# Performance work log

Measured on AMD Instinct MI355X. Metric: run time of the kernel, lower is better.

## Reference

```python
import jax, jax.numpy as jnp
import numpy as np

N = 32768
D_IN = 1728   # 192*3*3
D = 1024
C_CLS = 2


def setup_inputs() -> dict:
    key = jax.random.key(0)
    ks = jax.random.split(key, 8)
    # _initialize_weights: Linear weights ~ N(0, 0.01), biases zero
    x = jax.random.normal(ks[0], (N, D_IN), dtype=jnp.float32)
    w1 = jax.random.normal(ks[1], (D, D_IN), dtype=jnp.float32) * 0.01
    b1 = jnp.zeros((D,), jnp.float32)
    w2 = jax.random.normal(ks[2], (D, D), dtype=jnp.float32) * 0.01
    b2 = jnp.zeros((D,), jnp.float32)
    w_fc = jax.random.normal(ks[3], (C_CLS, D), dtype=jnp.float32) * 0.01
    b_fc = jnp.zeros((C_CLS,), jnp.float32)
    w_q = jax.random.normal(ks[4], (D, D), dtype=jnp.float32) * 0.01
    b_q = jnp.zeros((D,), jnp.float32)
    w_v = jax.random.normal(ks[5], (D, D), dtype=jnp.float32) * 0.01
    b_v = jnp.zeros((D,), jnp.float32)
    # Conv1d(2,2,kernel_size=1024): weight [out=2, in=2, k=1024]
    fan = C_CLS * D
    w_fcc = jax.random.uniform(ks[6], (C_CLS, C_CLS, D), jnp.float32,
                               -1.0 / np.sqrt(fan), 1.0 / np.sqrt(fan))
    b_fcc = jax.random.uniform(ks[7], (C_CLS,), jnp.float32,
                               -1.0 / np.sqrt(fan), 1.0 / np.sqrt(fan))
    return {"x": x, "w1": w1, "b1": b1, "w2": w2, "b2": b2,
            "w_fc": w_fc, "b_fc": b_fc, "w_q": w_q, "b_q": b_q,
            "w_v": w_v, "b_v": b_v, "w_fcc": w_fcc, "b_fcc": b_fcc}


def reference(x, w1, b1, w2, b2, w_fc, b_fc, w_q, b_q, w_v, b_v, w_fcc, b_fcc):
    # classifier MLP (dropout = identity in eval)
    h = jax.nn.relu(x @ w1.T + b1)          # [N, 1024]
    feat = jax.nn.relu(h @ w2.T + b2)       # [N, 1024]
    instance_pred = feat @ w_fc.T + b_fc    # [N, 2]
    V = feat @ w_v.T + b_v                  # [N, 1024]
    Q = feat @ w_q.T + b_q                  # [N, 1024]
    # torch.sort(..., descending=True)[1][0] == argmax per class column
    top_idx = jnp.argmax(instance_pred, axis=0)   # [2]
    m_feats = feat[top_idx]                 # [2, 1024]
    q_max = m_feats @ w_q.T + b_q           # [2, 1024]
    scale = jnp.sqrt(jnp.float32(Q.shape[1]))
    A = jax.nn.softmax((Q @ q_max.T) / scale, axis=0)  # softmax over instances, [N, 2]
    B = A.T @ V                             # [2, 1024]
    # Conv1d(2,2,k=1024) over length-1024 input -> single output position
    C = (jnp.einsum('oik,ik->o', w_fcc, B) + b_fcc).reshape(1, C_CLS)
    return instance_pred, C, A, B[None]
```

## Files before the change

### kernel.cpp

```cpp
#include <hip/hip_runtime.h>
#include <stdint.h>


typedef unsigned short u16;
typedef __attribute__((ext_vector_type(8))) short short8;
typedef __attribute__((ext_vector_type(4))) float floatx4;

#define TILE 128
#define BK 32

__device__ __forceinline__ float bf2f(u16 u) {
  union { unsigned u; float f; } x; x.u = ((unsigned)u) << 16; return x.f;
}
__device__ __forceinline__ u16 f2bf(float f) {
  union { float f; unsigned u; } x; x.f = f;
  return (u16)((x.u + 0x7fffu + ((x.u >> 16) & 1u)) >> 16);
}
__device__ __forceinline__ unsigned ordf(float f) {
  union { float f; unsigned u; } x; x.f = f;
  return (x.u & 0x80000000u) ? ~x.u : (x.u | 0x80000000u);
}
__device__ __forceinline__ void gload16(const void* g, void* l) {
  __builtin_amdgcn_global_load_lds(
      (const __attribute__((address_space(1))) void*)g,
      (__attribute__((address_space(3))) void*)l, 16, 0, 0);
}

template <int MODE>
__global__ __launch_bounds__(256) void gemm_bt(
    const u16* __restrict__ A, const u16* __restrict__ B,
    const float* __restrict__ bias, u16* __restrict__ O,
    float* __restrict__ OL, int K, int ntiles, int ldo) {
  __shared__ __align__(16) u16 SH[16384];

  const int xcd = blockIdx.x & 7;
  const int j = blockIdx.x >> 3;
  const int mstride = gridDim.x / (ntiles << 3);
  const int mt = xcd * mstride + j / ntiles;
  const int nt = j % ntiles;
  const int m0 = mt * TILE, n0 = nt * TILE;
  const int tid = threadIdx.x;
  const int lane = tid & 63;
  const int wm = (tid >> 7) * 64;
  const int wn = ((tid >> 6) & 1) * 64;

  floatx4 acc[4][4];
#pragma unroll
  for (int i = 0; i < 4; ++i)
#pragma unroll
    for (int jf = 0; jf < 4; ++jf) acc[i][jf] = (floatx4){0.f, 0.f, 0.f, 0.f};

  const int srow = tid >> 2;
  const int sq = ((tid & 3) - srow) & 3;
  const u16* Ag0 = A + (size_t)(m0 + srow) * K + sq * 8;
  const u16* Ag1 = Ag0 + (size_t)64 * K;
  const u16* Bg0 = B + (size_t)(n0 + srow) * K + sq * 8;
  const u16* Bg1 = Bg0 + (size_t)64 * K;
  u16* const ASl[2] = {SH + tid * 8, SH + 4096 + tid * 8};
  u16* const BSl[2] = {SH + 8192 + tid * 8, SH + 12288 + tid * 8};

  const int fr = lane & 15;
  const int fq = lane >> 4;
  const int fo = (size_t)0;
  const u16* const AF[2] = {
      SH + (wm + fr) * BK + (((fq + fr) & 3) * 8),
      SH + 4096 + (wm + fr) * BK + (((fq + fr) & 3) * 8)};
  const u16* const BF[2] = {
      SH + 8192 + (wn + fr) * BK + (((fq + fr) & 3) * 8),
      SH + 12288 + (wn + fr) * BK + (((fq + fr) & 3) * 8)};
  (void)fo;

  gload16(Ag0, ASl[0]); gload16(Ag1, ASl[0] + 2048);
  gload16(Bg0, BSl[0]); gload16(Bg1, BSl[0] + 2048);
  Ag0 += BK; Ag1 += BK; Bg0 += BK; Bg1 += BK;

  const int kiters = K / BK;
  for (int kt = 0; kt < kiters; ++kt) {
    const int cur = kt & 1, nxt = cur ^ 1;
    __syncthreads();
    if (kt + 1 < kiters) {
      gload16(Ag0, ASl[nxt]); gload16(Ag1, ASl[nxt] + 2048);
      gload16(Bg0, BSl[nxt]); gload16(Bg1, BSl[nxt] + 2048);
      Ag0 += BK; Ag1 += BK; Bg0 += BK; Bg1 += BK;
    }
    short8 a[4], b[4];
#pragma unroll
    for (int f = 0; f < 4; ++f) {
      a[f] = *(const short8*)(AF[cur] + f * 16 * BK);
      b[f] = *(const short8*)(BF[cur] + f * 16 * BK);
    }
#pragma unroll
    for (int i = 0; i < 4; ++i)
#pragma unroll
      for (int jf = 0; jf < 4; ++jf)
        acc[i][jf] = __builtin_amdgcn_mfma_f32_16x16x32_bf16(a[i], b[jf],
                                                             acc[i][jf], 0, 0, 0);
  }

  const int er = fq * 4;
  const int ec = fr;
  if (MODE == 1 && n0 >= 1024) {
    if (wn == 0 && ec < 2) {
#pragma unroll
      for (int i = 0; i < 4; ++i) {
        const int row = m0 + wm + i * 16 + er;
#pragma unroll
        for (int r = 0; r < 4; ++r)
          OL[(size_t)(row + r) * 2 + ec] = acc[i][0][r];
      }
    }
    return;
  }

  __syncthreads();
#pragma unroll
  for (int jf = 0; jf < 4; ++jf) {
    const int col = wn + jf * 16 + ec;
    const float bv = bias[n0 + col];
#pragma unroll
    for (int i = 0; i < 4; ++i) {
      const int row = wm + i * 16 + er;
#pragma unroll
      for (int r = 0; r < 4; ++r) {
        float v = acc[i][jf][r] + bv;
        if (MODE == 0) v = fmaxf(v, 0.f);
        SH[(row + r) * TILE + col] = f2bf(v);
      }
    }
  }
  __syncthreads();
#pragma unroll
  for (int c = 0; c < 8; ++c) {
    const int flat = c * 256 + tid;
    const int row = flat >> 4, ch = flat & 15;
    short8 v = *(const short8*)(SH + flat * 8);
    *(short8*)(O + (size_t)(m0 + row) * ldo + n0 + ch * 8) = v;
  }
}

__global__ void k_prep(const float* __restrict__ x, const float* __restrict__ w1,
                       const float* __restrict__ w2, const float* __restrict__ wv,
                       u16* __restrict__ XB, u16* __restrict__ W1B,
                       u16* __restrict__ W2B, u16* __restrict__ B3,
                       float* __restrict__ Bbuf, unsigned long long* __restrict__ keys) {
  int b = blockIdx.x;
  const int tid = threadIdx.x;
  const float* s; u16* d;
  if (b < 55296) { s = x; d = XB; }
  else if ((b -= 55296) < 1728) { s = w1; d = W1B; }
  else if ((b -= 1728) < 1024) { s = w2; d = W2B; }
  else if ((b -= 1024) < 1024) { s = wv; d = B3; }
  else {
    b -= 1024;
    int i = b * 256 + tid;
    if (i < 129024) B3[1026 * 1024 + i] = 0;
    if (i < 2048) Bbuf[i] = 0.f;
    if (i < 2) keys[i] = 0ull;
    return;
  }
  int i = b * 256 + tid;
  float4 v = ((const float4*)s)[i];
  unsigned long long o = (unsigned long long)f2bf(v.x) |
                         ((unsigned long long)f2bf(v.y) << 16) |
                         ((unsigned long long)f2bf(v.z) << 32) |
                         ((unsigned long long)f2bf(v.w) << 48);
  ((unsigned long long*)d)[i] = o;
}

__global__ __launch_bounds__(256) void k_ip(const u16* __restrict__ feat,
                                            const float* __restrict__ wfc,
                                            const float* __restrict__ bfc,
                                            float* __restrict__ out_ip) {
  const int row = blockIdx.x * 4 + (threadIdx.x >> 6);
  const int lane = threadIdx.x & 63;
  const u16* fr = feat + (size_t)row * 1024 + lane * 16;
  const float* w0 = wfc + lane * 16;
  const float* w1 = wfc + 1024 + lane * 16;
  float s0 = 0.f, s1 = 0.f;
#pragma unroll
  for (int t = 0; t < 16; ++t) {
    float f = bf2f(fr[t]);
    s0 += f * w0[t];
    s1 += f * w1[t];
  }
#pragma unroll
  for (int off = 32; off > 0; off >>= 1) {
    s0 += __shfl_down(s0, off, 64);
    s1 += __shfl_down(s1, off, 64);
  }
  if (lane == 0) {
    out_ip[(size_t)row * 2 + 0] = s0 + bfc[0];
    out_ip[(size_t)row * 2 + 1] = s1 + bfc[1];
  }
}

__global__ __launch_bounds__(256) void k_argmax(const float* __restrict__ ip,
                                                unsigned long long* __restrict__ keys) {
  float m0 = -1e30f, m1 = -1e30f;
  int i0 = 0, i1 = 0;
  for (int i = blockIdx.x * 256 + threadIdx.x; i < 32768; i += 256 * 64) {
    float v0 = ip[2 * i], v1 = ip[2 * i + 1];
    if (v0 > m0) { m0 = v0; i0 = i; }
    if (v1 > m1) { m1 = v1; i1 = i; }
  }
  unsigned long long k0 =
      ((unsigned long long)ordf(m0) << 32) | (0xFFFFFFFFu - (unsigned)i0);
  unsigned long long k1 =
      ((unsigned long long)ordf(m1) << 32) | (0xFFFFFFFFu - (unsigned)i1);
#pragma unroll
  for (int off = 32; off > 0; off >>= 1) {
    unsigned long long t0 = __shfl_down(k0, off, 64);
    unsigned long long t1 = __shfl_down(k1, off, 64);
    if (t0 > k0) k0 = t0;
    if (t1 > k1) k1 = t1;
  }
  __shared__ unsigned long long s0[4], s1[4];
  const int lane = threadIdx.x & 63, wv = threadIdx.x >> 6;
  if (lane == 0) { s0[wv] = k0; s1[wv] = k1; }
  __syncthreads();
  if (threadIdx.x == 0) {
    for (int w = 1; w < 4; ++w) {
      if (s0[w] > k0) k0 = s0[w];
      if (s1[w] > k1) k1 = s1[w];
    }
    atomicMax(keys + 0, k0);
    atomicMax(keys + 1, k1);
  }
}

__global__ __launch_bounds__(256) void k_qmax(const u16* __restrict__ feat,
                                              const float* __restrict__ wq,
                                              const float* __restrict__ bq,
                                              const unsigned long long* __restrict__ keys,
                                              float* __restrict__ qmax) {
  const int gw = blockIdx.x * 4 + (threadIdx.x >> 6);
  const int c = gw >> 10, k = gw & 1023;
  const int lane = threadIdx.x & 63;
  const int idx = (int)(0xFFFFFFFFu - (unsigned)(keys[c] & 0xFFFFFFFFull));
  const u16* fr = feat + (size_t)idx * 1024 + lane * 16;
  const float* wr = wq + (size_t)k * 1024 + lane * 16;
  float s = 0.f;
#pragma unroll
  for (int t = 0; t < 16; ++t) s += bf2f(fr[t]) * wr[t];
#pragma unroll
  for (int off = 32; off > 0; off >>= 1) s += __shfl_down(s, off, 64);
  if (lane == 0) qmax[c * 1024 + k] = s + bq[k];
}

__global__ __launch_bounds__(256) void k_t(const float* __restrict__ wq,
                                           const float* __restrict__ qmax,
                                           float* __restrict__ tpart) {
  const int jb = blockIdx.x & 3, kp = blockIdx.x >> 2;
  const int jcol = jb * 256 + threadIdx.x;
  float s0 = 0.f, s1 = 0.f;
  for (int k = kp * 128; k < kp * 128 + 128; ++k) {
    float w = wq[(size_t)k * 1024 + jcol];
    s0 += qmax[k] * w;
    s1 += qmax[1024 + k] * w;
  }
  tpart[kp * 2048 + jcol] = s0;
  tpart[kp * 2048 + 1024 + jcol] = s1;
}

__global__ __launch_bounds__(256) void k_tcast(const float* __restrict__ tpart,
                                               u16* __restrict__ b3) {
  const int i = blockIdx.x * 256 + threadIdx.x;
  float s = 0.f;
#pragma unroll
  for (int kp = 0; kp < 8; ++kp) s += tpart[kp * 2048 + i];
  b3[(size_t)(1024 + (i >> 10)) * 1024 + (i & 1023)] = f2bf(s);
}

__global__ __launch_bounds__(256) void k_reduce(const float* __restrict__ lg,
                                                float* __restrict__ ms) {
  __shared__ float r0[256], r1[256];
  const int tid = threadIdx.x;
  float m0 = -1e30f, m1 = -1e30f;
  for (int i = tid; i < 32768; i += 256) {
    m0 = fmaxf(m0, lg[2 * i]);
    m1 = fmaxf(m1, lg[2 * i + 1]);
  }
  r0[tid] = m0; r1[tid] = m1;
  __syncthreads();
  for (int s = 128; s > 0; s >>= 1) {
    if (tid < s) {
      r0[tid] = fmaxf(r0[tid], r0[tid + s]);
      r1[tid] = fmaxf(r1[tid], r1[tid + s]);
    }
    __syncthreads();
  }
  m0 = r0[0]; m1 = r1[0];
  __syncthreads();
  float s0 = 0.f, s1 = 0.f;
  for (int i = tid; i < 32768; i += 256) {
    s0 += __expf((lg[2 * i] - m0) * 0.03125f);
    s1 += __expf((lg[2 * i + 1] - m1) * 0.03125f);
  }
  r0[tid] = s0; r1[tid] = s1;
  __syncthreads();
  for (int s = 128; s > 0; s >>= 1) {
    if (tid < s) { r0[tid] += r0[tid + s]; r1[tid] += r1[tid + s]; }
    __syncthreads();
  }
  if (tid == 0) { ms[0] = m0; ms[1] = m1; ms[2] = r0[0]; ms[3] = r1[0]; }
}

__global__ __launch_bounds__(256) void k_ab(const float* __restrict__ lg,
                                            const float* __restrict__ ms,
                                            const u16* __restrict__ V,
                                            float* __restrict__ outA,
                                            float* __restrict__ Bbuf) {
  const int tid = threadIdx.x;
  const int row0 = blockIdx.x * 128;
  const float m0 = ms[0], m1 = ms[1];
  const float inv0 = 1.f / ms[2], inv1 = 1.f / ms[3];
  {
    const int r = row0 + (tid >> 1);
    const int c = tid & 1;
    outA[2 * r + c] =
        __expf((lg[2 * r + c] - (c ? m1 : m0)) * 0.03125f) * (c ? inv1 : inv0);
  }
  float p0[4] = {0, 0, 0, 0}, p1[4] = {0, 0, 0, 0};
  const int kb = tid * 4;
  for (int r = row0; r < row0 + 128; ++r) {
    const float a0 = __expf((lg[2 * r] - m0) * 0.03125f) * inv0;
    const float a1 = __expf((lg[2 * r + 1] - m1) * 0.03125f) * inv1;
    unsigned long long vv = *(const unsigned long long*)(V + (size_t)r * 1024 + kb);
    float f0 = bf2f((u16)vv), f1 = bf2f((u16)(vv >> 16));
    float f2 = bf2f((u16)(vv >> 32)), f3 = bf2f((u16)(vv >> 48));
    p0[0] += a0 * f0; p0[1] += a0 * f1; p0[2] += a0 * f2; p0[3] += a0 * f3;
    p1[0] += a1 * f0; p1[1] += a1 * f1; p1[2] += a1 * f2; p1[3] += a1 * f3;
  }
#pragma unroll
  for (int t = 0; t < 4; ++t) {
    atomicAdd(&Bbuf[kb + t], p0[t]);
    atomicAdd(&Bbuf[1024 + kb + t], p1[t]);
  }
}

__global__ __launch_bounds__(256) void k_c(const float* __restrict__ Bbuf,
                                           const float* __restrict__ wfcc,
                                           const float* __restrict__ bfcc,
                                           float* __restrict__ outC,
                                           float* __restrict__ outB) {
  __shared__ float r0[256], r1[256];
  const int tid = threadIdx.x;
  float s0 = 0.f, s1 = 0.f;
  for (int i = tid; i < 2048; i += 256) {
    float b = Bbuf[i];
    outB[i] = b;
    s0 += wfcc[i] * b;
    s1 += wfcc[2048 + i] * b;
  }
  r0[tid] = s0; r1[tid] = s1;
  __syncthreads();
  for (int s = 128; s > 0; s >>= 1) {
    if (tid < s) { r0[tid] += r0[tid + s]; r1[tid] += r1[tid + s]; }
    __syncthreads();
  }
  if (tid == 0) {
    outC[0] = r0[0] + bfcc[0];
    outC[1] = r1[0] + bfcc[1];
  }
}

extern "C" void kernel_launch(void* const* d_in, const int* in_sizes, int n_in,
                              void* d_out, int out_size, void* d_ws, size_t ws_size,
                              hipStream_t stream) {
  const float* x    = (const float*)d_in[0];
  const float* w1   = (const float*)d_in[1];
  const float* b1   = (const float*)d_in[2];
  const float* w2   = (const float*)d_in[3];
  const float* b2   = (const float*)d_in[4];
  const float* wfc  = (const float*)d_in[5];
  const float* bfc  = (const float*)d_in[6];
  const float* wq   = (const float*)d_in[7];
  const float* bq   = (const float*)d_in[8];
  const float* wv   = (const float*)d_in[9];
  const float* bv   = (const float*)d_in[10];
  const float* wfcc = (const float*)d_in[11];
  const float* bfcc = (const float*)d_in[12];

  float* out   = (float*)d_out;
  float* outIP = out;
  float* outC  = out + 65536;
  float* outA  = out + 65538;
  float* outB  = out + 131074;

  char* ws = (char*)d_ws;
  u16* XB  = (u16*)(ws);
  u16* HB  = (u16*)(ws + 113246208);
  u16* FB  = (u16*)(ws + 180355072);
  u16* W1B = (u16*)(ws + 247463936);
  float* TPART = (float*)(ws + 247463936);
  u16* W2B = (u16*)(ws + 251002880);
  u16* B3  = (u16*)(ws + 253100032);
  float* LG = (float*)(ws + 255459328);
  float* QM = (float*)(ws + 255721472);
  unsigned long long* KEYS = (unsigned long long*)(ws + 255729664);
  float* MS   = (float*)(ws + 255729680);
  float* BBUF = (float*)(ws + 255729696);

  k_prep<<<55296 + 1728 + 1024 + 1024 + 505, 256, 0, stream>>>(
      x, w1, w2, wv, XB, W1B, W2B, B3, BBUF, KEYS);

  gemm_bt<0><<<256 * 8, 256, 0, stream>>>(XB, W1B, b1, HB, nullptr, 1728, 8, 1024);
  gemm_bt<0><<<256 * 8, 256, 0, stream>>>(HB, W2B, b2, FB, nullptr, 1024, 8, 1024);

  k_ip<<<8192, 256, 0, stream>>>(FB, wfc, bfc, outIP);
  k_argmax<<<64, 256, 0, stream>>>(outIP, KEYS);
  k_qmax<<<512, 256, 0, stream>>>(FB, wq, bq, KEYS, QM);
  k_t<<<32, 256, 0, stream>>>(wq, QM, TPART);
  k_tcast<<<8, 256, 0, stream>>>(TPART, B3);

  gemm_bt<1><<<256 * 9, 256, 0, stream>>>(FB, B3, bv, HB, LG, 1024, 9, 1024);

  k_reduce<<<1, 256, 0, stream>>>(LG, MS);
  k_ab<<<256, 256, 0, stream>>>(LG, MS, HB, outA, BBUF);
  k_c<<<1, 256, 0, stream>>>(BBUF, wfcc, bfcc, outC, outB);
}
```

Measured before the change: 923.7 us.

## Switch GEMM to single-buffered BK=64 tiles without LDS swizzle

Raises the K-tile depth from 32 to 64 and replaces the double-buffered LDS prefetch with a single buffer that is loaded, synchronised, consumed in two MFMA halves, then synchronised again. It also drops the XOR-style column swizzle on LDS stores and fragment reads. The goal is fewer loop iterations and barriers per unit of K work. In exchange, global loads no longer overlap with MFMA compute, and the unswizzled 128-byte row stride may cause LDS bank conflicts on fragment reads.

```diff
diff --git a/kernel.cpp b/kernel.cpp
--- a/kernel.cpp
+++ b/kernel.cpp
@@ -7,7 +7,7 @@
 typedef __attribute__((ext_vector_type(4))) float floatx4;
 
 #define TILE 128
-#define BK 32
+#define BK 64
 
 __device__ __forceinline__ float bf2f(u16 u) {
   union { unsigned u; float f; } x; x.u = ((unsigned)u) << 16; return x.f;
@@ -32,6 +32,8 @@
     const float* __restrict__ bias, u16* __restrict__ O,
     float* __restrict__ OL, int K, int ntiles, int ldo) {
   __shared__ __align__(16) u16 SH[16384];
+  u16* const As = SH;
+  u16* const Bs = SH + 8192;
 
   const int xcd = blockIdx.x & 7;
   const int j = blockIdx.x >> 3;
@@ -50,51 +52,43 @@
 #pragma unroll
     for (int jf = 0; jf < 4; ++jf) acc[i][jf] = (floatx4){0.f, 0.f, 0.f, 0.f};
 
-  const int srow = tid >> 2;
-  const int sq = ((tid & 3) - srow) & 3;
-  const u16* Ag0 = A + (size_t)(m0 + srow) * K + sq * 8;
-  const u16* Ag1 = Ag0 + (size_t)64 * K;
-  const u16* Bg0 = B + (size_t)(n0 + srow) * K + sq * 8;
-  const u16* Bg1 = Bg0 + (size_t)64 * K;
-  u16* const ASl[2] = {SH + tid * 8, SH + 4096 + tid * 8};
-  u16* const BSl[2] = {SH + 8192 + tid * 8, SH + 12288 + tid * 8};
+  const int trow = tid >> 3;
+  const int tch = tid & 7;
+  const u16* Ag = A + (size_t)(m0 + trow) * K + tch * 8;
+  const u16* Bg = B + (size_t)(n0 + trow) * K + tch * 8;
+  u16* const Al = As + tid * 8;
+  u16* const Bl = Bs + tid * 8;
 
   const int fr = lane & 15;
   const int fq = lane >> 4;
-  const int fo = (size_t)0;
-  const u16* const AF[2] = {
-      SH + (wm + fr) * BK + (((fq + fr) & 3) * 8),
-      SH + 4096 + (wm + fr) * BK + (((fq + fr) & 3) * 8)};
-  const u16* const BF[2] = {
-      SH + 8192 + (wn + fr) * BK + (((fq + fr) & 3) * 8),
-      SH + 12288 + (wn + fr) * BK + (((fq + fr) & 3) * 8)};
-  (void)fo;
-
-  gload16(Ag0, ASl[0]); gload16(Ag1, ASl[0] + 2048);
-  gload16(Bg0, BSl[0]); gload16(Bg1, BSl[0] + 2048);
-  Ag0 += BK; Ag1 += BK; Bg0 += BK; Bg1 += BK;
+  const u16* const Af = As + (wm + fr) * BK + fq * 8;
+  const u16* const Bf = Bs + (wn + fr) * BK + fq * 8;
 
   const int kiters = K / BK;
   for (int kt = 0; kt < kiters; ++kt) {
-    const int cur = kt & 1, nxt = cur ^ 1;
+#pragma unroll
+    for (int rd = 0; rd < 4; ++rd) {
+      gload16(Ag + (size_t)rd * 32 * K, Al + rd * 2048);
+      gload16(Bg + (size_t)rd * 32 * K, Bl + rd * 2048);
+    }
+    Ag += BK; Bg += BK;
     __syncthreads();
-    if (kt + 1 < kiters) {
-      gload16(Ag0, ASl[nxt]); gload16(Ag1, ASl[nxt] + 2048);
-      gload16(Bg0, BSl[nxt]); gload16(Bg1, BSl[nxt] + 2048);
-      Ag0 += BK; Ag1 += BK; Bg0 += BK; Bg1 += BK;
-    }
-    short8 a[4], b[4];
-#pragma unroll
-    for (int f = 0; f < 4; ++f) {
-      a[f] = *(const short8*)(AF[cur] + f * 16 * BK);
-      b[f] = *(const short8*)(BF[cur] + f * 16 * BK);
-    }
-#pragma unroll
-    for (int i = 0; i < 4; ++i)
-#pragma unroll
-      for (int jf = 0; jf < 4; ++jf)
-        acc[i][jf] = __builtin_amdgcn_mfma_f32_16x16x32_bf16(a[i], b[jf],
-                                                             acc[i][jf], 0, 0, 0);
+#pragma unroll
+    for (int h = 0; h < 2; ++h) {
+      short8 a[4], b[4];
+#pragma unroll
+      for (int f = 0; f < 4; ++f) {
+        a[f] = *(const short8*)(Af + f * 16 * BK + h * 32);
+        b[f] = *(const short8*)(Bf + f * 16 * BK + h * 32);
+      }
+#pragma unroll
+      for (int i = 0; i < 4; ++i)
+#pragma unroll
+        for (int jf = 0; jf < 4; ++jf)
+          acc[i][jf] = __builtin_amdgcn_mfma_f32_16x16x32_bf16(
+              a[i], b[jf], acc[i][jf], 0, 0, 0);
+    }
+    __syncthreads();
   }
 
   const int er = fq * 4;
@@ -112,7 +106,6 @@
     return;
   }
 
-  __syncthreads();
 #pragma unroll
   for (int jf = 0; jf < 4; ++jf) {
     const int col = wn + jf * 16 + ec;
```

Result: faster. 893.5 us (-3.3%).
